# Kernel optimization log

Measured on AMD Instinct MI355X. Metric: run time of the kernel, lower is better.

Reference implementation:

```python
import jax, jax.numpy as jnp
import numpy as np

H = 4096          # hidden_size
NIN = 17          # RFSIZE*RFSIZE + ADDINPUT + NBACTIONS = 9+4+4
NA = 4            # NBACTIONS


def setup_inputs() -> dict:
    key = jax.random.key(0)
    ks = jax.random.split(key, 12)
    return {
        "x": jax.random.normal(ks[0], (1, NIN), jnp.float32),
        "hidden": 0.1 * jax.random.normal(ks[1], (1, H), jnp.float32),
        "hebb": 0.01 * jax.random.normal(ks[2], (H, H), jnp.float32),
        "i2h_w": 0.1 * jax.random.normal(ks[3], (H, NIN), jnp.float32),
        "i2h_b": 0.1 * jax.random.normal(ks[4], (H,), jnp.float32),
        "w": 0.01 * jax.random.uniform(ks[5], (H, H), jnp.float32),
        "alpha": 0.01 * jax.random.uniform(ks[6], (H, H), jnp.float32),
        "eta": 0.01 * jnp.ones((1,), jnp.float32),
        "h2o_w": 0.1 * jax.random.normal(ks[7], (NA, H), jnp.float32),
        "h2o_b": 0.1 * jax.random.normal(ks[8], (NA,), jnp.float32),
        "h2v_w": 0.1 * jax.random.normal(ks[9], (1, H), jnp.float32),
        "h2v_b": 0.1 * jax.random.normal(ks[10], (1,), jnp.float32),
    }


def reference(x, hidden, hebb, i2h_w, i2h_b, w, alpha, eta, h2o_w, h2o_b, h2v_w, h2v_b):
    # plastic RNN step: h = tanh(i2h(x) + hidden @ (w + alpha*hebb))
    h = jnp.tanh(x @ i2h_w.T + i2h_b + hidden @ (w + alpha * hebb))  # [1,H]
    # Hebbian trace update: (1-eta)*hebb + eta * outer(hidden, h)
    hebb_new = (1.0 - eta) * hebb + eta * (hidden[0][:, None] * h[0][None, :])  # [H,H]
    activout = jax.nn.softmax(h @ h2o_w.T + h2o_b, axis=-1)  # [1,NA]
    valueout = h @ h2v_w.T + h2v_b                           # [1,1]
    return activout, valueout, h, hebb_new
```

## Files before the change

kernel.cpp:

```cpp
#include <hip/hip_runtime.h>

#define HDIM 4096
#define NIN 17
#define NA 4

constexpr int TB = 256;
constexpr int CPT = 4;
constexpr int BXC = HDIM / (TB * CPT);
constexpr int NCHUNK = 256;
constexpr int RPC = HDIM / NCHUNK;

__global__ __launch_bounds__(TB)
void k_matvec(const float* __restrict__ w, const float* __restrict__ alpha,
              const float* __restrict__ hebb, const float* __restrict__ hidden,
              float* __restrict__ partial) {
    const int col0 = (blockIdx.x * TB + threadIdx.x) * CPT;
    const int row0 = blockIdx.y * RPC;
    float4 acc = make_float4(0.f, 0.f, 0.f, 0.f);
#pragma unroll 4
    for (int r = 0; r < RPC; ++r) {
        const int i = row0 + r;
        const size_t off = (size_t)i * HDIM + col0;
        const float hv = hidden[i];
        const float4 wv = *(const float4*)(w + off);
        const float4 av = *(const float4*)(alpha + off);
        const float4 bv = *(const float4*)(hebb + off);
        acc.x += hv * (wv.x + av.x * bv.x);
        acc.y += hv * (wv.y + av.y * bv.y);
        acc.z += hv * (wv.z + av.z * bv.z);
        acc.w += hv * (wv.w + av.w * bv.w);
    }
    *(float4*)(partial + (size_t)blockIdx.y * HDIM + col0) = acc;
}

__global__ __launch_bounds__(256)
void k_hact(const float* __restrict__ partial,
            const float* __restrict__ x, const float* __restrict__ i2h_w,
            const float* __restrict__ i2h_b,
            float* __restrict__ h_f, float* __restrict__ h_out) {
    const int j = blockIdx.x * 256 + threadIdx.x;
    float s = 0.f;
    for (int c = 0; c < NCHUNK; ++c) s += partial[(size_t)c * HDIM + j];
    float z = i2h_b[j] + s;
#pragma unroll
    for (int k = 0; k < NIN; ++k) z += x[k] * i2h_w[j * NIN + k];
    const float h = tanhf(z);
    h_f[j] = h;
    h_out[j] = h;
}

__global__ __launch_bounds__(256)
void k_hebb(const float* __restrict__ hebb, const float* __restrict__ hidden,
            const float* __restrict__ h_f, const float* __restrict__ eta,
            float* __restrict__ hebb_out) {
    const size_t m = ((size_t)blockIdx.x * 256 + threadIdx.x) * 4;
    const float e = eta[0];
    const float om = 1.f - e;
    const int i = (int)(m >> 12);
    const int j = (int)(m & (HDIM - 1));
    const float hv = e * hidden[i];
    const float4 hb = *(const float4*)(hebb + m);
    const float4 hj = *(const float4*)(h_f + j);
    hebb_out[m]     = om * hb.x + hv * hj.x;
    hebb_out[m + 1] = om * hb.y + hv * hj.y;
    hebb_out[m + 2] = om * hb.z + hv * hj.z;
    hebb_out[m + 3] = om * hb.w + hv * hj.w;
}

__global__ __launch_bounds__(256)
void k_heads(const float* __restrict__ h_f,
             const float* __restrict__ h2o_w, const float* __restrict__ h2o_b,
             const float* __restrict__ h2v_w, const float* __restrict__ h2v_b,
             float* __restrict__ out) {
    const int tid = threadIdx.x;
    float acc[NA + 1] = {0.f, 0.f, 0.f, 0.f, 0.f};
    for (int t = 0; t < HDIM / 256; ++t) {
        const int j = t * 256 + tid;
        const float hv = h_f[j];
#pragma unroll
        for (int a = 0; a < NA; ++a) acc[a] += hv * h2o_w[a * HDIM + j];
        acc[NA] += hv * h2v_w[j];
    }
    __shared__ float red[256];
    __shared__ float res[NA + 1];
    for (int a = 0; a < NA + 1; ++a) {
        red[tid] = acc[a];
        __syncthreads();
        for (int sft = 128; sft > 0; sft >>= 1) {
            if (tid < sft) red[tid] += red[tid + sft];
            __syncthreads();
        }
        if (tid == 0) res[a] = red[0];
        __syncthreads();
    }
    if (tid == 0) {
        float o[NA];
        float mx = -1e30f;
        for (int a = 0; a < NA; ++a) { o[a] = res[a] + h2o_b[a]; mx = fmaxf(mx, o[a]); }
        float se = 0.f;
        for (int a = 0; a < NA; ++a) { o[a] = __expf(o[a] - mx); se += o[a]; }
        for (int a = 0; a < NA; ++a) out[a] = o[a] / se;
        out[NA] = res[NA] + h2v_b[0];
    }
}

extern "C" void kernel_launch(void* const* d_in, const int* in_sizes, int n_in,
                              void* d_out, int out_size, void* d_ws, size_t ws_size,
                              hipStream_t stream) {
    const float* x      = (const float*)d_in[0];
    const float* hidden = (const float*)d_in[1];
    const float* hebb   = (const float*)d_in[2];
    const float* i2h_w  = (const float*)d_in[3];
    const float* i2h_b  = (const float*)d_in[4];
    const float* w      = (const float*)d_in[5];
    const float* alpha  = (const float*)d_in[6];
    const float* eta    = (const float*)d_in[7];
    const float* h2o_w  = (const float*)d_in[8];
    const float* h2o_b  = (const float*)d_in[9];
    const float* h2v_w  = (const float*)d_in[10];
    const float* h2v_b  = (const float*)d_in[11];
    float* out = (float*)d_out;

    float* partial = (float*)d_ws;
    float* h_f = partial + (size_t)NCHUNK * HDIM;

    float* h_out    = out + 5;
    float* hebb_out = out + 5 + HDIM;

    k_matvec<<<dim3(BXC, NCHUNK), TB, 0, stream>>>(w, alpha, hebb, hidden, partial);
    k_hact<<<HDIM / 256, 256, 0, stream>>>(partial, x, i2h_w, i2h_b, h_f, h_out);
    k_hebb<<<(int)(((size_t)HDIM * HDIM) / 1024), 256, 0, stream>>>(hebb, hidden, h_f, eta, hebb_out);
    k_heads<<<1, 256, 0, stream>>>(h_f, h2o_w, h2o_b, h2v_w, h2v_b, out);
}
```

Before: 268.0 us.

## Fuse output heads into activation kernel and align hebb output stores

Computes the policy/value head dot products inside k_hact with per-block shared reductions and global atomics, replacing the single-block heads kernel with a tiny finishing kernel. Realigns the hebb update so each thread writes an aligned float4 to the output, which sits at an odd offset, with a scalar prologue and tail. Also bumps matvec unroll and adds occupancy hints. Atomic accumulation adds nondeterministic summation order.

```diff
diff --git a/kernel.cpp b/kernel.cpp
--- a/kernel.cpp
+++ b/kernel.cpp
@@ -9,22 +9,28 @@
 constexpr int BXC = HDIM / (TB * CPT);
 constexpr int NCHUNK = 256;
 constexpr int RPC = HDIM / NCHUNK;
+constexpr size_t NELEM = (size_t)HDIM * HDIM;
 
-__global__ __launch_bounds__(TB)
+__global__ __launch_bounds__(TB, 4)
 void k_matvec(const float* __restrict__ w, const float* __restrict__ alpha,
               const float* __restrict__ hebb, const float* __restrict__ hidden,
-              float* __restrict__ partial) {
+              float* __restrict__ partial, float* __restrict__ acc5) {
+    if (blockIdx.x == 0 && blockIdx.y == 0 && threadIdx.x < 8) acc5[threadIdx.x] = 0.f;
+
     const int col0 = (blockIdx.x * TB + threadIdx.x) * CPT;
     const int row0 = blockIdx.y * RPC;
+    const size_t base = (size_t)row0 * HDIM + col0;
+    const float* __restrict__ wp = w + base;
+    const float* __restrict__ ap = alpha + base;
+    const float* __restrict__ bp = hebb + base;
     float4 acc = make_float4(0.f, 0.f, 0.f, 0.f);
-#pragma unroll 4
+#pragma unroll 8
     for (int r = 0; r < RPC; ++r) {
-        const int i = row0 + r;
-        const size_t off = (size_t)i * HDIM + col0;
-        const float hv = hidden[i];
-        const float4 wv = *(const float4*)(w + off);
-        const float4 av = *(const float4*)(alpha + off);
-        const float4 bv = *(const float4*)(hebb + off);
+        const float hv = hidden[row0 + r];
+        const size_t off = (size_t)r * HDIM;
+        const float4 wv = *(const float4*)(wp + off);
+        const float4 av = *(const float4*)(ap + off);
+        const float4 bv = *(const float4*)(bp + off);
         acc.x += hv * (wv.x + av.x * bv.x);
         acc.y += hv * (wv.y + av.y * bv.y);
         acc.z += hv * (wv.z + av.z * bv.z);
@@ -34,12 +40,15 @@
 }
 
 __global__ __launch_bounds__(256)
-void k_hact(const float* __restrict__ partial,
-            const float* __restrict__ x, const float* __restrict__ i2h_w,
-            const float* __restrict__ i2h_b,
-            float* __restrict__ h_f, float* __restrict__ h_out) {
-    const int j = blockIdx.x * 256 + threadIdx.x;
+void k_hact(const float* __restrict__ partial, const float* __restrict__ x,
+            const float* __restrict__ i2h_w, const float* __restrict__ i2h_b,
+            const float* __restrict__ h2o_w, const float* __restrict__ h2v_w,
+            float* __restrict__ h_f, float* __restrict__ h_out,
+            float* __restrict__ acc5) {
+    const int tid = threadIdx.x;
+    const int j = blockIdx.x * 256 + tid;
     float s = 0.f;
+#pragma unroll 16
     for (int c = 0; c < NCHUNK; ++c) s += partial[(size_t)c * HDIM + j];
     float z = i2h_b[j] + s;
 #pragma unroll
@@ -47,60 +56,79 @@
     const float h = tanhf(z);
     h_f[j] = h;
     h_out[j] = h;
+
+    float d[NA + 1];
+#pragma unroll
+    for (int a = 0; a < NA; ++a) d[a] = h * h2o_w[(size_t)a * HDIM + j];
+    d[NA] = h * h2v_w[j];
+
+    __shared__ float red[256];
+#pragma unroll
+    for (int a = 0; a < NA + 1; ++a) {
+        red[tid] = d[a];
+        __syncthreads();
+        for (int sft = 128; sft > 0; sft >>= 1) {
+            if (tid < sft) red[tid] += red[tid + sft];
+            __syncthreads();
+        }
+        if (tid == 0) atomicAdd(acc5 + a, red[0]);
+        __syncthreads();
+    }
 }
 
 __global__ __launch_bounds__(256)
 void k_hebb(const float* __restrict__ hebb, const float* __restrict__ hidden,
             const float* __restrict__ h_f, const float* __restrict__ eta,
             float* __restrict__ hebb_out) {
-    const size_t m = ((size_t)blockIdx.x * 256 + threadIdx.x) * 4;
+    const size_t t = (size_t)blockIdx.x * 256 + threadIdx.x;
+    const size_t s = 4 * t + 3;
     const float e = eta[0];
     const float om = 1.f - e;
-    const int i = (int)(m >> 12);
-    const int j = (int)(m & (HDIM - 1));
-    const float hv = e * hidden[i];
-    const float4 hb = *(const float4*)(hebb + m);
-    const float4 hj = *(const float4*)(h_f + j);
-    hebb_out[m]     = om * hb.x + hv * hj.x;
-    hebb_out[m + 1] = om * hb.y + hv * hj.y;
-    hebb_out[m + 2] = om * hb.z + hv * hj.z;
-    hebb_out[m + 3] = om * hb.w + hv * hj.w;
+
+    if (t == 0) {
+        const float hv0 = e * hidden[0];
+        hebb_out[0] = om * hebb[0] + hv0 * h_f[0];
+        hebb_out[1] = om * hebb[1] + hv0 * h_f[1];
+        hebb_out[2] = om * hebb[2] + hv0 * h_f[2];
+    }
+
+    if (s + 3 < NELEM) {
+        const float b0 = hebb[s];
+        const float4 bv = *(const float4*)(hebb + s + 1);
+        const float b[4] = {b0, bv.x, bv.y, bv.z};
+        float v[4];
+#pragma unroll
+        for (int k = 0; k < 4; ++k) {
+            const size_t m = s + (size_t)k;
+            const int i = (int)(m >> 12);
+            const int jj = (int)(m & (HDIM - 1));
+            v[k] = om * b[k] + e * hidden[i] * h_f[jj];
+        }
+        *(float4*)(hebb_out + s) = make_float4(v[0], v[1], v[2], v[3]);
+    } else {
+        for (size_t m = s; m < NELEM; ++m) {
+            const int i = (int)(m >> 12);
+            const int jj = (int)(m & (HDIM - 1));
+            hebb_out[m] = om * hebb[m] + e * hidden[i] * h_f[jj];
+        }
+    }
 }
 
-__global__ __launch_bounds__(256)
-void k_heads(const float* __restrict__ h_f,
-             const float* __restrict__ h2o_w, const float* __restrict__ h2o_b,
-             const float* __restrict__ h2v_w, const float* __restrict__ h2v_b,
-             float* __restrict__ out) {
-    const int tid = threadIdx.x;
-    float acc[NA + 1] = {0.f, 0.f, 0.f, 0.f, 0.f};
-    for (int t = 0; t < HDIM / 256; ++t) {
-        const int j = t * 256 + tid;
-        const float hv = h_f[j];
-#pragma unroll
-        for (int a = 0; a < NA; ++a) acc[a] += hv * h2o_w[a * HDIM + j];
-        acc[NA] += hv * h2v_w[j];
-    }
-    __shared__ float red[256];
-    __shared__ float res[NA + 1];
-    for (int a = 0; a < NA + 1; ++a) {
-        red[tid] = acc[a];
-        __syncthreads();
-        for (int sft = 128; sft > 0; sft >>= 1) {
-            if (tid < sft) red[tid] += red[tid + sft];
-            __syncthreads();
-        }
-        if (tid == 0) res[a] = red[0];
-        __syncthreads();
-    }
-    if (tid == 0) {
+__global__ __launch_bounds__(64)
+void k_finish(const float* __restrict__ acc5,
+              const float* __restrict__ h2o_b, const float* __restrict__ h2v_b,
+              float* __restrict__ out) {
+    if (threadIdx.x == 0) {
         float o[NA];
         float mx = -1e30f;
-        for (int a = 0; a < NA; ++a) { o[a] = res[a] + h2o_b[a]; mx = fmaxf(mx, o[a]); }
+#pragma unroll
+        for (int a = 0; a < NA; ++a) { o[a] = acc5[a] + h2o_b[a]; mx = fmaxf(mx, o[a]); }
         float se = 0.f;
+#pragma unroll
         for (int a = 0; a < NA; ++a) { o[a] = __expf(o[a] - mx); se += o[a]; }
+#pragma unroll
         for (int a = 0; a < NA; ++a) out[a] = o[a] / se;
-        out[NA] = res[NA] + h2v_b[0];
+        out[NA] = acc5[NA] + h2v_b[0];
     }
 }
 
@@ -122,13 +150,14 @@
     float* out = (float*)d_out;
 
     float* partial = (float*)d_ws;
-    float* h_f = partial + (size_t)NCHUNK * HDIM;
+    float* h_f  = partial + (size_t)NCHUNK * HDIM;
+    float* acc5 = h_f + HDIM;
 
     float* h_out    = out + 5;
     float* hebb_out = out + 5 + HDIM;
 
-    k_matvec<<<dim3(BXC, NCHUNK), TB, 0, stream>>>(w, alpha, hebb, hidden, partial);
-    k_hact<<<HDIM / 256, 256, 0, stream>>>(partial, x, i2h_w, i2h_b, h_f, h_out);
-    k_hebb<<<(int)(((size_t)HDIM * HDIM) / 1024), 256, 0, stream>>>(hebb, hidden, h_f, eta, hebb_out);
-    k_heads<<<1, 256, 0, stream>>>(h_f, h2o_w, h2o_b, h2v_w, h2v_b, out);
+    k_matvec<<<dim3(BXC, NCHUNK), TB, 0, stream>>>(w, alpha, hebb, hidden, partial, acc5);
+    k_hact<<<HDIM / 256, 256, 0, stream>>>(partial, x, i2h_w, i2h_b, h2o_w, h2v_w, h_f, h_out, acc5);
+    k_hebb<<<(int)((NELEM / 4) / 256), 256, 0, stream>>>(hebb, hidden, h_f, eta, hebb_out);
+    k_finish<<<1, 64, 0, stream>>>(acc5, h2o_b, h2v_b, out);
 }
```

Result: no change. 272.3 us (+1.6%).
